# Kernel tuning notes

Hardware: AMD Instinct MI355X
Metric: run time of the kernel (lower is better)

The kernel has to match this reference:

```python
import jax, jax.numpy as jnp
import numpy as np

NEG_SLOPE = 0.2  # PyG GATConv default negative_slope


def gat_conv(x, edge_index, W, att_src, att_dst, bias):
    # PyG GATConv, heads=1, add_self_loops=True, lin bias=False, final bias added
    N = x.shape[0]
    h = x @ W                                     # [N, F]
    loops = jnp.arange(N, dtype=edge_index.dtype)
    src = jnp.concatenate([edge_index[0], loops])
    dst = jnp.concatenate([edge_index[1], loops])
    a_src = h @ att_src                           # [N]
    a_dst = h @ att_dst                           # [N]
    e = a_src[src] + a_dst[dst]
    e = jnp.where(e > 0, e, NEG_SLOPE * e)        # leaky_relu
    m = jax.ops.segment_max(e, dst, num_segments=N)
    w = jnp.exp(e - m[dst])
    denom = jax.ops.segment_sum(w, dst, num_segments=N)
    alpha = w / denom[dst]
    out = jax.ops.segment_sum(h[src] * alpha[:, None], dst, num_segments=N)
    return out + bias


def gcn_conv(x, edge_index, W, b):
    # PyG GCNConv: add self-loops + symmetric normalization
    N = x.shape[0]
    loops = jnp.arange(N, dtype=edge_index.dtype)
    src = jnp.concatenate([edge_index[0], loops])
    dst = jnp.concatenate([edge_index[1], loops])
    deg = jax.ops.segment_sum(jnp.ones(src.shape[0], dtype=x.dtype), dst, num_segments=N)
    dinv = jax.lax.rsqrt(jnp.maximum(deg, 1e-12))  # deg >= 1 thanks to self-loops
    norm = dinv[src] * dinv[dst]
    xw = x @ W
    return jax.ops.segment_sum(xw[src] * norm[:, None], dst, num_segments=N) + b


def get_final_node(x, batch, num_graphs):
    nn_ = jax.ops.segment_sum(jnp.ones(x.shape[0], dtype=jnp.int32), batch, num_segments=num_graphs)
    cum = jnp.concatenate([jnp.zeros(1, dtype=nn_.dtype), jnp.cumsum(nn_)[:-1]])
    return x[cum]


def ontology_emb(table, e1, e2, W, asrc, adst, b, idx_map):
    emb = gat_conv(table, e1, W, asrc, adst, b)
    emb = gat_conv(emb, e2, W, asrc, adst, b)
    return emb[idx_map]


def _forward(spec_emb, diag_table, proce_table, atc_table,
             diag_W, diag_asrc, diag_adst, diag_b,
             proce_W, proce_asrc, proce_adst, proce_b,
             atc_W, atc_asrc, atc_adst, atc_b,
             gcn_W1, gcn_b1, gcn_W2, gcn_b2, gcn_W3, gcn_b3,
             diag_e1, diag_e2, proce_e1, proce_e2, atc_e1, atc_e2,
             diag_map, proce_map, atc_map,
             left_x, left_graph_index, right_x, right_graph_index,
             left_x_batch, right_x_batch, num_graphs):
    diag_emb = ontology_emb(diag_table, diag_e1, diag_e2, diag_W, diag_asrc, diag_adst, diag_b, diag_map)
    proce_emb = ontology_emb(proce_table, proce_e1, proce_e2, proce_W, proce_asrc, proce_adst, proce_b, proce_map)
    atc_emb = ontology_emb(atc_table, atc_e1, atc_e2, atc_W, atc_asrc, atc_adst, atc_b, atc_map)
    all_emb = jnp.concatenate([spec_emb, diag_emb, proce_emb, atc_emb], axis=0)
    lh = all_emb[left_x[:, 0]]   # squeeze(dim=1)
    rh = all_emb[right_x[:, 0]]
    for W, b in ((gcn_W1, gcn_b1), (gcn_W2, gcn_b2), (gcn_W3, gcn_b3)):
        lh = gcn_conv(lh, left_graph_index, W, b)
        rh = gcn_conv(rh, right_graph_index, W, b)
    lf = get_final_node(lh, left_x_batch, num_graphs)
    rf = get_final_node(rh, right_x_batch, num_graphs)
    eps = 1e-6  # CosineSimilarity eps
    num = jnp.sum(lf * rf, axis=-1)
    den = jnp.maximum(jnp.linalg.norm(lf, axis=-1), eps) * jnp.maximum(jnp.linalg.norm(rf, axis=-1), eps)
    return num / den


def setup_inputs() -> dict:
    key = jax.random.key(0)
    ks = jax.random.split(key, 32)
    HID = 128
    B, NPG = 2048, 50
    N = B * NPG               # 102400 nodes per side
    E_PAT = 409600            # 4 edges per node
    DIAG_N, DIAG_L = 30000, 20000
    PROCE_N, PROCE_L = 12000, 8000
    ATC_N, ATC_L = 6000, 4000
    ALL = 1 + DIAG_L + PROCE_L + ATC_L
    f = lambda k, s: jax.random.normal(k, s, dtype=jnp.float32)
    scale = 0.1
    inp = {
        'spec_emb': f(ks[0], (1, HID)),
        'diag_table': f(ks[1], (DIAG_N, HID)),
        'proce_table': f(ks[2], (PROCE_N, HID)),
        'atc_table': f(ks[3], (ATC_N, HID)),
    }
    for i, nm in enumerate(['diag', 'proce', 'atc']):
        inp[nm + '_W'] = f(ks[4 + i], (HID, HID)) * scale
        inp[nm + '_asrc'] = f(ks[7 + i], (HID,)) * scale
        inp[nm + '_adst'] = f(ks[10 + i], (HID,)) * scale
        inp[nm + '_b'] = jnp.zeros((HID,), jnp.float32)
    for j in range(3):
        inp['gcn_W%d' % (j + 1)] = f(ks[13 + j], (HID, HID)) * scale
        inp['gcn_b%d' % (j + 1)] = jnp.zeros((HID,), jnp.float32)
    inp['diag_e1'] = jax.random.randint(ks[16], (2, DIAG_N), 0, DIAG_N, dtype=jnp.int32)
    inp['diag_e2'] = jax.random.randint(ks[17], (2, DIAG_N), 0, DIAG_N, dtype=jnp.int32)
    inp['proce_e1'] = jax.random.randint(ks[18], (2, PROCE_N), 0, PROCE_N, dtype=jnp.int32)
    inp['proce_e2'] = jax.random.randint(ks[19], (2, PROCE_N), 0, PROCE_N, dtype=jnp.int32)
    inp['atc_e1'] = jax.random.randint(ks[20], (2, ATC_N), 0, ATC_N, dtype=jnp.int32)
    inp['atc_e2'] = jax.random.randint(ks[21], (2, ATC_N), 0, ATC_N, dtype=jnp.int32)
    inp['diag_map'] = jnp.arange(DIAG_L, dtype=jnp.int32)
    inp['proce_map'] = jnp.arange(PROCE_L, dtype=jnp.int32)
    inp['atc_map'] = jnp.arange(ATC_L, dtype=jnp.int32)
    inp['left_x'] = jax.random.randint(ks[22], (N, 1), 0, ALL, dtype=jnp.int32)
    inp['right_x'] = jax.random.randint(ks[23], (N, 1), 0, ALL, dtype=jnp.int32)
    inp['left_graph_index'] = jax.random.randint(ks[24], (2, E_PAT), 0, N, dtype=jnp.int32)
    inp['right_graph_index'] = jax.random.randint(ks[25], (2, E_PAT), 0, N, dtype=jnp.int32)
    batch = jnp.repeat(jnp.arange(B, dtype=jnp.int32), NPG)
    inp['left_x_batch'] = batch
    inp['right_x_batch'] = batch
    inp['num_graphs'] = B
    return inp


def reference(spec_emb, diag_table, proce_table, atc_table,
              diag_W, diag_asrc, diag_adst, diag_b,
              proce_W, proce_asrc, proce_adst, proce_b,
              atc_W, atc_asrc, atc_adst, atc_b,
              gcn_W1, gcn_b1, gcn_W2, gcn_b2, gcn_W3, gcn_b3,
              diag_e1, diag_e2, proce_e1, proce_e2, atc_e1, atc_e2,
              diag_map, proce_map, atc_map,
              left_x, left_graph_index, right_x, right_graph_index,
              left_x_batch, right_x_batch, num_graphs):
    return _forward(spec_emb, diag_table, proce_table, atc_table,
                    diag_W, diag_asrc, diag_adst, diag_b,
                    proce_W, proce_asrc, proce_adst, proce_b,
                    atc_W, atc_asrc, atc_adst, atc_b,
                    gcn_W1, gcn_b1, gcn_W2, gcn_b2, gcn_W3, gcn_b3,
                    diag_e1, diag_e2, proce_e1, proce_e2, atc_e1, atc_e2,
                    diag_map, proce_map, atc_map,
                    left_x, left_graph_index, right_x, right_graph_index,
                    left_x_batch, right_x_batch, num_graphs)
```

## Files before the change

### kernel.cpp

```cpp
#include <hip/hip_runtime.h>
#include <hip/hip_bf16.h>

#define HID 128

typedef unsigned int uint;
typedef unsigned short ushort;
typedef short short8 __attribute__((ext_vector_type(8)));
typedef float f32x4 __attribute__((ext_vector_type(4)));

static inline int cdiv_i(long a, long b) { return (int)((a + b - 1) / b); }
static inline int imax_i(int a, int b) { return a > b ? a : b; }

__device__ __forceinline__ float bf2f(uint hi) {
    return __builtin_bit_cast(float, hi << 16);
}
__device__ __forceinline__ ushort f2bf(float f) {
    uint u = __builtin_bit_cast(uint, f);
    u = (u + 0x7fffu + ((u >> 16) & 1u)) >> 16;
    return (ushort)u;
}

struct CsrDesc {
    const int* esrc[8];
    const int* edst[8];
    int ebase[9];
    int nbase[9];
    int totE;
};

__device__ __forceinline__ void stage_wt(const ushort* __restrict__ Wt,
                                         ushort* __restrict__ wl) {
    const int t = threadIdx.x;
    const int row = t >> 1, half = (t & 1) * 64;
    const uint4* src = (const uint4*)(Wt + row * 128 + half);
    uint4* dst = (uint4*)(wl + row * 136 + half);
#pragma unroll
    for (int i = 0; i < 8; ++i) dst[i] = src[i];
}

template <typename AT>
__device__ __forceinline__ void load_afrag(const AT* __restrict__ A, long row,
                                           int koff, short8& af) {
    if constexpr (__is_same(AT, ushort)) {
        const uint4 raw = *(const uint4*)(A + row * 128 + koff);
        af = __builtin_bit_cast(short8, raw);
    } else {
        const float4* p = (const float4*)(A + row * 128 + koff);
        const float4 x0 = p[0], x1 = p[1];
        af[0] = (short)f2bf(x0.x); af[1] = (short)f2bf(x0.y);
        af[2] = (short)f2bf(x0.z); af[3] = (short)f2bf(x0.w);
        af[4] = (short)f2bf(x1.x); af[5] = (short)f2bf(x1.y);
        af[6] = (short)f2bf(x1.z); af[7] = (short)f2bf(x1.w);
    }
}

struct GOnto {
    const ushort* Wt0; const ushort* Wt1; const ushort* Wt2;
    const float* s0; const float* s1; const float* s2;
    const float* d0; const float* d1; const float* d2;
    int bs1, bs2;
    int r1, r2, r3;
};

template <typename AT>
__device__ void gemm_onto_dev(int b, const AT* __restrict__ x0,
                              const AT* __restrict__ x1, const AT* __restrict__ x2,
                              const GOnto& g, ushort* __restrict__ H,
                              float* __restrict__ as_o, float* __restrict__ ad_o,
                              ushort* __restrict__ wl) {
    const int gid = (b >= g.bs1) + (b >= g.bs2);
    const ushort* Wt = (gid == 0) ? g.Wt0 : (gid == 1) ? g.Wt1 : g.Wt2;
    const float* avs = (gid == 0) ? g.s0 : (gid == 1) ? g.s1 : g.s2;
    const float* avd = (gid == 0) ? g.d0 : (gid == 1) ? g.d1 : g.d2;
    const AT* Ag = (gid == 0) ? x0 : (gid == 1) ? x1 : x2;
    const int bloc = b - ((gid == 0) ? 0 : (gid == 1) ? g.bs1 : g.bs2);
    const long rb = (gid == 0) ? 0 : (gid == 1) ? g.r1 : g.r2;
    const long Mg = ((gid == 0) ? g.r1 : (gid == 1) ? g.r2 : g.r3) - rb;
    stage_wt(Wt, wl);
    __syncthreads();

    const int tid = threadIdx.x;
    const int wave = tid >> 6, lane = tid & 63;
    const int r = lane & 15, q = lane >> 4;
    const long m0 = (long)bloc * 128 + wave * 32;

    f32x4 acc[2][8];
#pragma unroll
    for (int mi = 0; mi < 2; ++mi)
#pragma unroll
        for (int ni = 0; ni < 8; ++ni) acc[mi][ni] = (f32x4)0.f;

#pragma unroll
    for (int t = 0; t < 4; ++t) {
        const int koff = t * 32 + q * 8;
        short8 bfr[8];
#pragma unroll
        for (int ni = 0; ni < 8; ++ni) {
            const uint4 raw = *(const uint4*)(&wl[(ni * 16 + r) * 136 + koff]);
            bfr[ni] = __builtin_bit_cast(short8, raw);
        }
#pragma unroll
        for (int mi = 0; mi < 2; ++mi) {
            long row = m0 + mi * 16 + r;
            if (row >= Mg) row = Mg - 1;
            short8 af;
            load_afrag<AT>(Ag, row, koff, af);
#pragma unroll
            for (int ni = 0; ni < 8; ++ni)
                acc[mi][ni] = __builtin_amdgcn_mfma_f32_16x16x32_bf16(
                    af, bfr[ni], acc[mi][ni], 0, 0, 0);
        }
    }

    ushort* Hg = H + rb * 128;
#pragma unroll
    for (int mi = 0; mi < 2; ++mi) {
#pragma unroll
        for (int ni = 0; ni < 8; ++ni) {
            const int col = ni * 16 + r;
#pragma unroll
            for (int reg = 0; reg < 4; ++reg) {
                const long row = m0 + mi * 16 + q * 4 + reg;
                if (row < Mg) Hg[row * 128 + col] = f2bf(acc[mi][ni][reg]);
            }
        }
    }

    float asv[8], adv[8];
#pragma unroll
    for (int ni = 0; ni < 8; ++ni) {
        asv[ni] = avs[ni * 16 + r];
        adv[ni] = avd[ni * 16 + r];
    }
#pragma unroll
    for (int mi = 0; mi < 2; ++mi) {
#pragma unroll
        for (int reg = 0; reg < 4; ++reg) {
            float ps = 0.f, pd = 0.f;
#pragma unroll
            for (int ni = 0; ni < 8; ++ni) {
                ps += acc[mi][ni][reg] * asv[ni];
                pd += acc[mi][ni][reg] * adv[ni];
            }
#pragma unroll
            for (int o = 1; o < 16; o <<= 1) {
                ps += __shfl_xor(ps, o);
                pd += __shfl_xor(pd, o);
            }
            const long row = m0 + mi * 16 + q * 4 + reg;
            if (r == 0 && row < Mg) {
                as_o[rb + row] = ps;
                ad_o[rb + row] = pd;
            }
        }
    }
}

__global__ __launch_bounds__(256) void gemm_onto_l2(const ushort* __restrict__ x0,
                                                    const ushort* __restrict__ x1,
                                                    const ushort* __restrict__ x2,
                                                    GOnto g, ushort* __restrict__ H,
                                                    float* __restrict__ as_o,
                                                    float* __restrict__ ad_o) {
    __shared__ ushort wl[128 * 136];
    gemm_onto_dev<ushort>(blockIdx.x, x0, x1, x2, g, H, as_o, ad_o, wl);
}

struct EmbSrc {
    const float* spec; const ushort* oE;
    const int* m0; const int* m1; const int* m2;
    int lb2, lb3, r1, r2;
};

__device__ __forceinline__ short8 load_emb(const EmbSrc& e, long row, int koff) {
    short8 af;
    if (row == 0) {
        const float4* pp = (const float4*)(e.spec + koff);
        const float4 x0 = pp[0], x1 = pp[1];
        af[0] = (short)f2bf(x0.x); af[1] = (short)f2bf(x0.y);
        af[2] = (short)f2bf(x0.z); af[3] = (short)f2bf(x0.w);
        af[4] = (short)f2bf(x1.x); af[5] = (short)f2bf(x1.y);
        af[6] = (short)f2bf(x1.z); af[7] = (short)f2bf(x1.w);
        return af;
    }
    const int r = (int)row;
    const int seg = (r >= e.lb2) + (r >= e.lb3);
    const int local = r - ((seg == 0) ? 1 : (seg == 1) ? e.lb2 : e.lb3);
    const int* mp = (seg == 0) ? e.m0 : (seg == 1) ? e.m1 : e.m2;
    const int rb = (seg == 0) ? 0 : (seg == 1) ? e.r1 : e.r2;
    const long sr = (long)rb + mp[local];
    return __builtin_bit_cast(short8, *(const uint4*)(e.oE + sr * 128 + koff));
}

__device__ void gemm_pat_tile(const EmbSrc& es, const ushort* __restrict__ wl,
                              ushort* __restrict__ C, long m0blk, long rowEnd) {
    const int tid = threadIdx.x;
    const int wave = tid >> 6, lane = tid & 63;
    const int r = lane & 15, q = lane >> 4;
    const long m0 = m0blk + wave * 32;

    f32x4 acc[2][8];
#pragma unroll
    for (int mi = 0; mi < 2; ++mi)
#pragma unroll
        for (int ni = 0; ni < 8; ++ni) acc[mi][ni] = (f32x4)0.f;

#pragma unroll
    for (int t = 0; t < 4; ++t) {
        const int koff = t * 32 + q * 8;
        short8 bfr[8];
#pragma unroll
        for (int ni = 0; ni < 8; ++ni) {
            const uint4 raw = *(const uint4*)(&wl[(ni * 16 + r) * 136 + koff]);
            bfr[ni] = __builtin_bit_cast(short8, raw);
        }
#pragma unroll
        for (int mi = 0; mi < 2; ++mi) {
            long row = m0 + mi * 16 + r;
            if (row >= rowEnd) row = rowEnd - 1;
            const short8 af = load_emb(es, row, koff);
#pragma unroll
            for (int ni = 0; ni < 8; ++ni)
                acc[mi][ni] = __builtin_amdgcn_mfma_f32_16x16x32_bf16(
                    af, bfr[ni], acc[mi][ni], 0, 0, 0);
        }
    }

#pragma unroll
    for (int mi = 0; mi < 2; ++mi) {
#pragma unroll
        for (int ni = 0; ni < 8; ++ni) {
            const int col = ni * 16 + r;
#pragma unroll
            for (int reg = 0; reg < 4; ++reg) {
                const long row = m0 + mi * 16 + q * 4 + reg;
                if (row < rowEnd) C[row * 128 + col] = f2bf(acc[mi][ni][reg]);
            }
        }
    }
}

__global__ __launch_bounds__(256) void gemm_pat(EmbSrc es,
                                                const ushort* __restrict__ Wt,
                                                ushort* __restrict__ C, int M) {
    __shared__ ushort wl[128 * 136];
    stage_wt(Wt, wl);
    __syncthreads();
    const long m0 = (long)blockIdx.x * 256;
    gemm_pat_tile(es, wl, C, m0, M);
    if (m0 + 128 < M) gemm_pat_tile(es, wl, C, m0 + 128, M);
}

__device__ __forceinline__ void fold1_dev(int idx, const float* __restrict__ W2,
                                          const float* __restrict__ b2,
                                          const float* __restrict__ W3,
                                          float* __restrict__ W23b) {
    if (idx >= 129 * 128) return;
    const int i = idx >> 7, j = idx & 127;
    const float* a = (i < 128) ? (W2 + i * 128) : b2;
    float s = 0.f;
#pragma unroll 8
    for (int k = 0; k < 128; ++k) s += a[k] * W3[k * 128 + j];
    W23b[idx] = s;
}

__device__ __forceinline__ void fold2_dev(int idx, const float* __restrict__ W1,
                                          const float* __restrict__ b1,
                                          const float* __restrict__ W23b,
                                          ushort* __restrict__ WpT,
                                          float* __restrict__ cbuf) {
    if (idx >= 130 * 128) return;
    const int i = idx >> 7, j = idx & 127;
    if (i == 129) { cbuf[128 + j] = W23b[128 * 128 + j]; return; }
    const float* a = (i < 128) ? (W1 + i * 128) : b1;
    float s = 0.f;
#pragma unroll 8
    for (int k = 0; k < 128; ++k) s += a[k] * W23b[k * 128 + j];
    if (i < 128) WpT[j * 128 + i] = f2bf(s);
    else cbuf[j] = s;
}

__device__ __forceinline__ void mark_dev(int i, const int* __restrict__ lEg,
                                         const int* __restrict__ rEg, int EP,
                                         int NP, int* __restrict__ mk,
                                         int testBit, int setBit) {
    int src, dst;
    if (i < 2 * EP) {
        const int side = i >= EP;
        const int e = i - side * EP;
        const int* eg = side ? rEg : lEg;
        src = side * NP + eg[e];
        dst = side * NP + eg[EP + e];
    } else if (i < 2 * EP + 2 * NP) {
        src = dst = i - 2 * EP;
    } else return;
    if (mk[dst] & testBit) atomicOr(&mk[src], setBit);
}

__device__ __forceinline__ void csr_count_dev(int i, const CsrDesc& d,
                                              int* __restrict__ cnt,
                                              int* __restrict__ pos) {
    if (i >= d.totE) return;
    int li = 0;
#pragma unroll
    for (int k = 1; k < 8; ++k) li += (i >= d.ebase[k]);
    const int v = d.nbase[li] + d.edst[li][i - d.ebase[li]];
    pos[i] = atomicAdd(&cnt[v], 1);
}

struct PackPrep {
    const float* W2; const float* b2; const float* W3; float* W23b;
    const float* wsrc[3]; ushort* wt_out;
    int* cnt; int NV;
    const int* bL; const int* bR; int NP;
    int* gfL; int* gfR; int* mk;
    int nbF1, nbWT, nbInit;
};

__global__ __launch_bounds__(256) void k_prep(PackPrep p) {
    const int b = blockIdx.x, tid = threadIdx.x;
    if (b < p.nbF1) {
        fold1_dev(b * 256 + tid, p.W2, p.b2, p.W3, p.W23b);
    } else if (b < p.nbF1 + p.nbWT) {
        const int idx = (b - p.nbF1) * 256 + tid;
        if (idx < 3 * 16384) {
            const int m = idx >> 14;
            const int e = idx & 16383;
            const int n = e >> 7, k = e & 127;
            p.wt_out[idx] = f2bf(p.wsrc[m][k * 128 + n]);
        }
    } else {
        const int i = (b - p.nbF1 - p.nbWT) * 256 + tid;
        if (i < p.NV) p.cnt[i] = 0;
        if (i < 2 * p.NP) {
            const int side = i >= p.NP;
            const int ii = i - (side ? p.NP : 0);
            const int* bb = side ? p.bR : p.bL;
            int* gf = side ? p.gfR : p.gfL;
            const int cur = bb[ii];
            const int prev = (ii == 0) ? -1 : bb[ii - 1];
            int m = 0;
            if (cur > prev) {
                for (int g = prev + 1; g <= cur; ++g) gf[g] = ii;
                m = 1;
            }
            p.mk[i] = m;
        }
    }
}

struct PackScatter {
    const float* W1; const float* b1; const float* W23b;
    ushort* WpT; float* cbuf;
    CsrDesc dsc; int* cnt; int* pos;
    const int* lEg; const int* rEg; int EP; int NP; int* mk;
    int nbF2, nbCnt, nbMark;
};

__global__ __launch_bounds__(256) void k_scatter(PackScatter p) {
    const int b = blockIdx.x, tid = threadIdx.x;
    if (b < p.nbF2) {
        fold2_dev(b * 256 + tid, p.W1, p.b1, p.W23b, p.WpT, p.cbuf);
    } else if (b < p.nbF2 + p.nbCnt) {
        csr_count_dev((b - p.nbF2) * 256 + tid, p.dsc, p.cnt, p.pos);
    } else {
        mark_dev((b - p.nbF2 - p.nbCnt) * 256 + tid, p.lEg, p.rEg, p.EP, p.NP,
                 p.mk, 1, 2);
    }
}

__device__ void scan_tile_dev(const int* __restrict__ in, int* __restrict__ out,
                              int* __restrict__ bsum, int n, int pn0, int pcnt,
                              float* __restrict__ dinv, int tb, int tid,
                              int* sbuf) {
    const int base = tb * 1024 + tid * 4;
    int v[4];
    int s = 0;
#pragma unroll
    for (int k = 0; k < 4; ++k) {
        const int i = base + k;
        v[k] = (i < n) ? (in[i] + 1) : 0;
        if (i >= pn0 && i < pn0 + pcnt)
            dinv[i - pn0] = rsqrtf(fmaxf((float)v[k], 1e-12f));
        s += v[k];
    }
    sbuf[tid] = s;
    __syncthreads();
    int x = s;
    for (int o = 1; o < 256; o <<= 1) {
        const int t = (tid >= o) ? sbuf[tid - o] : 0;
        __syncthreads();
        x += t;
        sbuf[tid] = x;
        __syncthreads();
    }
    int run = x - s;
#pragma unroll
    for (int k = 0; k < 4; ++k) {
        const int i = base + k;
        if (i < n) out[i] = run;
        run += v[k];
    }
    if (tid == 255) bsum[tb] = x;
}

struct PackMid {
    const float* x0; const float* x1; const float* x2;
    GOnto go; ushort* H; float* as_o; float* ad_o;
    const int* cnt; int* offs; int* bsum;
    int NV; int pn0; int pcnt; float* dinv;
    const int* lEg; const int* rEg; int EP; int NP; int* mk;
    int nbGemm, nbScan;
};

__global__ __launch_bounds__(256) void k_mid(PackMid p) {
    __shared__ uint smem4[128 * 136 / 2];
    const int b = blockIdx.x, tid = threadIdx.x;
    if (b < p.nbGemm) {
        gemm_onto_dev<float>(b, p.x0, p.x1, p.x2, p.go, p.H, p.as_o, p.ad_o,
                             (ushort*)smem4);
    } else if (b < p.nbGemm + p.nbScan) {
        scan_tile_dev(p.cnt, p.offs, p.bsum, p.NV, p.pn0, p.pcnt, p.dinv,
                      b - p.nbGemm, tid, (int*)smem4);
    } else {
        mark_dev((b - p.nbGemm - p.nbScan) * 256 + tid, p.lEg, p.rEg, p.EP,
                 p.NP, p.mk, 2, 4);
    }
}

__global__ __launch_bounds__(256) void k_scanfin(int* __restrict__ out,
                                                 const int* __restrict__ bsum,
                                                 int n, int nbData) {
    __shared__ int sbuf[256];
    const int tb = blockIdx.x, tid = threadIdx.x;
    int pLim = tb < nbData ? tb : nbData;
    int pth = 0;
    for (int j = tid; j < pLim; j += 256) pth += bsum[j];
    sbuf[tid] = pth;
    __syncthreads();
    for (int o = 128; o > 0; o >>= 1) {
        if (tid < o) sbuf[tid] += sbuf[tid + o];
        __syncthreads();
    }
    const int prefix = sbuf[0];
    const int base = tb * 1024 + tid * 4;
#pragma unroll
    for (int k = 0; k < 4; ++k) {
        const int i = base + k;
        if (i < n) out[i] += prefix;
        else if (i == n) out[i] = prefix + ((tb < nbData) ? bsum[tb] : 0);
    }
}

struct FillP {
    CsrDesc dsc;
    const int* offs; const int* pos; const int* cnt;
    int* srcl; int4* pedge; const float* dinv;
    const int* lx; const int* rx; const int* mk;
    int NP, pB;
    int eStart, eCount, vStart, vCount;
};

__device__ void fill_dev(const FillP& f, int idx) {
    int v, s, li, cidx;
    if (idx < f.eCount) {
        const int i = f.eStart + idx;
        li = 0;
#pragma unroll
        for (int k = 1; k < 8; ++k) li += (i >= f.dsc.ebase[k]);
        const int j = i - f.dsc.ebase[li];
        v = f.dsc.nbase[li] + f.dsc.edst[li][j];
        s = f.dsc.esrc[li][j];
        cidx = f.offs[v] + f.pos[i];
    } else if (idx < f.eCount + f.vCount) {
        v = f.vStart + (idx - f.eCount);
        li = 0;
#pragma unroll
        for (int k = 1; k < 8; ++k) li += (v >= f.dsc.nbase[k]);
        s = v - f.dsc.nbase[li];
        cidx = f.offs[v] + f.cnt[v];
    } else return;
    if (li >= 6) {
        const int n2l = v - f.dsc.nbase[6];
        if (f.mk[n2l] == 0) return;
        const int sg = (li - 6) * f.NP + s;
        int4 rec;
        rec.x = sg;
        rec.y = (li == 7 ? f.rx : f.lx)[s];
        rec.z = __float_as_int(f.dinv[n2l] * f.dinv[sg]);
        rec.w = 0;
        f.pedge[cidx - f.pB] = rec;
    } else {
        f.srcl[cidx] = s;
    }
}

__global__ __launch_bounds__(256) void k_fill(FillP f) {
    fill_dev(f, blockIdx.x * 256 + threadIdx.x);
}

struct GatP {
    int r1, r2;
    int ob0, ob1, ob2;
    const float* b0; const float* b1; const float* b2;
};

__device__ __forceinline__ void acc8(float* acc, float w, const uint4 v) {
    acc[0] += w * bf2f(v.x & 0xffff);
    acc[1] += w * bf2f(v.x >> 16);
    acc[2] += w * bf2f(v.y & 0xffff);
    acc[3] += w * bf2f(v.y >> 16);
    acc[4] += w * bf2f(v.z & 0xffff);
    acc[5] += w * bf2f(v.z >> 16);
    acc[6] += w * bf2f(v.w & 0xffff);
    acc[7] += w * bf2f(v.w >> 16);
}

__device__ void gat_dev(int node, int ql, const ushort* __restrict__ h,
                        const float* __restrict__ as, const float* __restrict__ ad,
                        const int* __restrict__ offs, const int* __restrict__ srcl,
                        const GatP& p, ushort* __restrict__ out, int Mtot) {
    if (node >= Mtot) return;
    const int gid = (node >= p.r1) + (node >= p.r2);
    const int rb = (gid == 0) ? 0 : (gid == 1) ? p.r1 : p.r2;
    const int ob = (gid == 0) ? p.ob0 : (gid == 1) ? p.ob1 : p.ob2;
    const float* bias = (gid == 0) ? p.b0 : (gid == 1) ? p.b1 : p.b2;
    const int local = node - rb;
    const int beg = offs[ob + local], end = offs[ob + local + 1];
    const float adv = ad[node];
    float m = -1e30f;
    for (int j = beg; j < end; ++j) {
        float e = as[rb + srcl[j]] + adv;
        e = (e > 0.f) ? e : 0.2f * e;
        m = fmaxf(m, e);
    }
    float denom = 0.f;
    float acc[8] = {0.f, 0.f, 0.f, 0.f, 0.f, 0.f, 0.f, 0.f};
    int j = beg;
    for (; j + 2 <= end; j += 2) {
        const int s0 = srcl[j], s1 = srcl[j + 1];
        float e0 = as[rb + s0] + adv; e0 = (e0 > 0.f) ? e0 : 0.2f * e0;
        float e1 = as[rb + s1] + adv; e1 = (e1 > 0.f) ? e1 : 0.2f * e1;
        const float w0 = __expf(e0 - m), w1 = __expf(e1 - m);
        const uint4 v0 = *(const uint4*)(h + (size_t)(rb + s0) * 128 + ql * 8);
        const uint4 v1 = *(const uint4*)(h + (size_t)(rb + s1) * 128 + ql * 8);
        denom += w0 + w1;
        acc8(acc, w0, v0);
        acc8(acc, w1, v1);
    }
    if (j < end) {
        const int s0 = srcl[j];
        float e0 = as[rb + s0] + adv; e0 = (e0 > 0.f) ? e0 : 0.2f * e0;
        const float w0 = __expf(e0 - m);
        const uint4 v0 = *(const uint4*)(h + (size_t)(rb + s0) * 128 + ql * 8);
        denom += w0;
        acc8(acc, w0, v0);
    }
    const float inv = 1.f / denom;
    const float4 bv0 = *(const float4*)(bias + ql * 8);
    const float4 bv1 = *(const float4*)(bias + ql * 8 + 4);
    uint4 o;
    o.x = (uint)f2bf(acc[0] * inv + bv0.x) | ((uint)f2bf(acc[1] * inv + bv0.y) << 16);
    o.y = (uint)f2bf(acc[2] * inv + bv0.z) | ((uint)f2bf(acc[3] * inv + bv0.w) << 16);
    o.z = (uint)f2bf(acc[4] * inv + bv1.x) | ((uint)f2bf(acc[5] * inv + bv1.y) << 16);
    o.w = (uint)f2bf(acc[6] * inv + bv1.z) | ((uint)f2bf(acc[7] * inv + bv1.w) << 16);
    *(uint4*)(out + (size_t)node * 128 + ql * 8) = o;
}

__global__ __launch_bounds__(256) void gat_all(const ushort* __restrict__ h,
                                               const float* __restrict__ as,
                                               const float* __restrict__ ad,
                                               const int* __restrict__ offs,
                                               const int* __restrict__ srcl,
                                               GatP p, ushort* __restrict__ out,
                                               int Mtot) {
    gat_dev(blockIdx.x * 16 + (threadIdx.x >> 4), threadIdx.x & 15, h, as, ad,
            offs, srcl, p, out, Mtot);
}

struct GatFill {
    const ushort* h; const float* as; const float* ad;
    const int* offs; const int* srcl;
    GatP gp; ushort* out; int Mtot; int nbGat;
    FillP f;
};

__global__ __launch_bounds__(256) void k_gat_fill(GatFill g) {
    const int b = blockIdx.x, tid = threadIdx.x;
    if (b < g.nbGat) {
        gat_dev(b * 16 + (tid >> 4), tid & 15, g.h, g.as, g.ad, g.offs, g.srcl,
                g.gp, g.out, g.Mtot);
    } else {
        fill_dev(g.f, (b - g.nbGat) * 256 + tid);
    }
}

__global__ __launch_bounds__(256) void gcn_agg1(const ushort* __restrict__ A3,
                                                const int4* __restrict__ pedge,
                                                const int* __restrict__ offs6,
                                                const float* __restrict__ c1,
                                                ushort* __restrict__ t1,
                                                const int* __restrict__ mk,
                                                int NP2, int pB) {
    const int n2 = blockIdx.x * 16 + (threadIdx.x >> 4);
    const int ql = threadIdx.x & 15;
    if (n2 >= NP2) return;
    if ((mk[n2] & 4) == 0) return;
    const int beg = offs6[n2] - pB, end = offs6[n2 + 1] - pB;
    float acc[8] = {0.f, 0.f, 0.f, 0.f, 0.f, 0.f, 0.f, 0.f};
    int j = beg;
    for (; j + 2 <= end; j += 2) {
        const int4 r0 = pedge[j], r1 = pedge[j + 1];
        const float w0 = __int_as_float(r0.z), w1 = __int_as_float(r1.z);
        const uint4 v0 = *(const uint4*)(A3 + (size_t)r0.y * 128 + ql * 8);
        const uint4 v1 = *(const uint4*)(A3 + (size_t)r1.y * 128 + ql * 8);
        acc8(acc, w0, v0);
        acc8(acc, w1, v1);
    }
    if (j < end) {
        const int4 r0 = pedge[j];
        const uint4 v0 = *(const uint4*)(A3 + (size_t)r0.y * 128 + ql * 8);
        acc8(acc, __int_as_float(r0.z), v0);
    }
    const float4 bv0 = *(const float4*)(c1 + ql * 8);
    const float4 bv1 = *(const float4*)(c1 + ql * 8 + 4);
    uint4 o;
    o.x = (uint)f2bf(acc[0] + bv0.x) | ((uint)f2bf(acc[1] + bv0.y) << 16);
    o.y = (uint)f2bf(acc[2] + bv0.z) | ((uint)f2bf(acc[3] + bv0.w) << 16);
    o.z = (uint)f2bf(acc[4] + bv1.x) | ((uint)f2bf(acc[5] + bv1.y) << 16);
    o.w = (uint)f2bf(acc[6] + bv1.z) | ((uint)f2bf(acc[7] + bv1.w) << 16);
    *(uint4*)(t1 + (size_t)n2 * 128 + ql * 8) = o;
}

__device__ __forceinline__ void gcn_q_acc(const ushort* __restrict__ x,
                                          const int4* __restrict__ pedge,
                                          int beg, int end, int ql, float* acc) {
    int j = beg;
    for (; j + 2 <= end; j += 2) {
        const int4 r0 = pedge[j], r1 = pedge[j + 1];
        const float w0 = __int_as_float(r0.z), w1 = __int_as_float(r1.z);
        const uint4 v0 = *(const uint4*)(x + (size_t)r0.x * 128 + ql * 8);
        const uint4 v1 = *(const uint4*)(x + (size_t)r1.x * 128 + ql * 8);
        acc8(acc, w0, v0);
        acc8(acc, w1, v1);
    }
    if (j < end) {
        const int4 r0 = pedge[j];
        const uint4 v0 = *(const uint4*)(x + (size_t)r0.x * 128 + ql * 8);
        acc8(acc, __int_as_float(r0.z), v0);
    }
}

__global__ __launch_bounds__(256) void gcn_agg2(const ushort* __restrict__ t1,
                                                const int4* __restrict__ pedge,
                                                const int* __restrict__ offs6,
                                                const float* __restrict__ c2,
                                                ushort* __restrict__ t2,
                                                const int* __restrict__ mk,
                                                int NP2, int pB) {
    const int n2 = blockIdx.x * 16 + (threadIdx.x >> 4);
    const int ql = threadIdx.x & 15;
    if (n2 >= NP2) return;
    if ((mk[n2] & 2) == 0) return;
    const int beg = offs6[n2] - pB, end = offs6[n2 + 1] - pB;
    float acc[8] = {0.f, 0.f, 0.f, 0.f, 0.f, 0.f, 0.f, 0.f};
    gcn_q_acc(t1, pedge, beg, end, ql, acc);
    const float4 bv0 = *(const float4*)(c2 + ql * 8);
    const float4 bv1 = *(const float4*)(c2 + ql * 8 + 4);
    uint4 o;
    o.x = (uint)f2bf(acc[0] + bv0.x) | ((uint)f2bf(acc[1] + bv0.y) << 16);
    o.y = (uint)f2bf(acc[2] + bv0.z) | ((uint)f2bf(acc[3] + bv0.w) << 16);
    o.z = (uint)f2bf(acc[4] + bv1.x) | ((uint)f2bf(acc[5] + bv1.y) << 16);
    o.w = (uint)f2bf(acc[6] + bv1.z) | ((uint)f2bf(acc[7] + bv1.w) << 16);
    *(uint4*)(t2 + (size_t)n2 * 128 + ql * 8) = o;
}

__global__ __launch_bounds__(256) void final_cos(const ushort* __restrict__ t2,
                                                 const int4* __restrict__ pedge,
                                                 const int* __restrict__ offs6,
                                                 const int* __restrict__ gfL,
                                                 const int* __restrict__ gfR,
                                                 const float* __restrict__ b3,
                                                 float* __restrict__ out,
                                                 int B, int NP, int pB) {
    const int g = blockIdx.x * 8 + (threadIdx.x >> 5);
    const int l32 = threadIdx.x & 31;
    const int side = l32 >> 4;
    const int ql = l32 & 15;
    if (g >= B) return;
    const int n2 = (side ? NP : 0) + (side ? gfR : gfL)[g];
    const int beg = offs6[n2] - pB, end = offs6[n2 + 1] - pB;
    float acc[8] = {0.f, 0.f, 0.f, 0.f, 0.f, 0.f, 0.f, 0.f};
    gcn_q_acc(t2, pedge, beg, end, ql, acc);
    const float4 bv0 = *(const float4*)(b3 + ql * 8);
    const float4 bv1 = *(const float4*)(b3 + ql * 8 + 4);
    float v[8];
    v[0] = acc[0] + bv0.x; v[1] = acc[1] + bv0.y;
    v[2] = acc[2] + bv0.z; v[3] = acc[3] + bv0.w;
    v[4] = acc[4] + bv1.x; v[5] = acc[5] + bv1.y;
    v[6] = acc[6] + bv1.z; v[7] = acc[7] + bv1.w;
    float num = 0.f, nself = 0.f, nother = 0.f;
#pragma unroll
    for (int j = 0; j < 8; ++j) {
        const float o = __shfl_xor(v[j], 16);
        num += v[j] * o;
        nself += v[j] * v[j];
        nother += o * o;
    }
#pragma unroll
    for (int o1 = 1; o1 < 16; o1 <<= 1) {
        num += __shfl_xor(num, o1);
        nself += __shfl_xor(nself, o1);
        nother += __shfl_xor(nother, o1);
    }
    if (l32 == 0)
        out[g] = num / (fmaxf(sqrtf(nself), 1e-6f) * fmaxf(sqrtf(nother), 1e-6f));
}

extern "C" void kernel_launch(void* const* d_in, const int* in_sizes, int n_in,
                              void* d_out, int out_size, void* d_ws, size_t ws_size,
                              hipStream_t stream) {
    (void)n_in; (void)ws_size;
    const float* spec = (const float*)d_in[0];
    const float* tabs[3] = {(const float*)d_in[1], (const float*)d_in[2], (const float*)d_in[3]};
    const float* ontW[3] = {(const float*)d_in[4], (const float*)d_in[8], (const float*)d_in[12]};
    const float* ontAs[3] = {(const float*)d_in[5], (const float*)d_in[9], (const float*)d_in[13]};
    const float* ontAd[3] = {(const float*)d_in[6], (const float*)d_in[10], (const float*)d_in[14]};
    const float* ontB[3] = {(const float*)d_in[7], (const float*)d_in[11], (const float*)d_in[15]};
    const float* gcnW[3] = {(const float*)d_in[16], (const float*)d_in[18], (const float*)d_in[20]};
    const float* gcnB[3] = {(const float*)d_in[17], (const float*)d_in[19], (const float*)d_in[21]};
    const int* e1s[3] = {(const int*)d_in[22], (const int*)d_in[24], (const int*)d_in[26]};
    const int* e2s[3] = {(const int*)d_in[23], (const int*)d_in[25], (const int*)d_in[27]};
    const int* maps[3] = {(const int*)d_in[28], (const int*)d_in[29], (const int*)d_in[30]};
    const int* left_x = (const int*)d_in[31];
    const int* right_x = (const int*)d_in[32];
    const int* left_eg = (const int*)d_in[33];
    const int* right_eg = (const int*)d_in[34];
    const int* left_batch = (const int*)d_in[35];
    const int* right_batch = (const int*)d_in[36];

    int Ms[3] = {in_sizes[1] / HID, in_sizes[2] / HID, in_sizes[3] / HID};
    int E1s[3] = {in_sizes[22] / 2, in_sizes[24] / 2, in_sizes[26] / 2};
    int E2s[3] = {in_sizes[23] / 2, in_sizes[25] / 2, in_sizes[27] / 2};
    int Ls[3] = {in_sizes[28], in_sizes[29], in_sizes[30]};
    const int NP = in_sizes[31];
    const int EP = in_sizes[33] / 2;
    const int B = out_size;
    const long ALL = 1 + (long)Ls[0] + Ls[1] + Ls[2];
    const int Mtot = Ms[0] + Ms[1] + Ms[2];
    const int r1 = Ms[0], r2 = Ms[0] + Ms[1];

    CsrDesc dsc;
    int eCnt[8], nCnt[8];
    for (int i = 0; i < 3; ++i) {
        dsc.esrc[2 * i] = e1s[i];     dsc.edst[2 * i] = e1s[i] + E1s[i];
        dsc.esrc[2 * i + 1] = e2s[i]; dsc.edst[2 * i + 1] = e2s[i] + E2s[i];
        eCnt[2 * i] = E1s[i]; eCnt[2 * i + 1] = E2s[i];
        nCnt[2 * i] = Ms[i];  nCnt[2 * i + 1] = Ms[i];
    }
    dsc.esrc[6] = left_eg;  dsc.edst[6] = left_eg + EP;  eCnt[6] = EP; nCnt[6] = NP;
    dsc.esrc[7] = right_eg; dsc.edst[7] = right_eg + EP; eCnt[7] = EP; nCnt[7] = NP;
    dsc.ebase[0] = 0;
    int nb_acc = 0;
    for (int i = 0; i < 8; ++i) {
        dsc.ebase[i + 1] = dsc.ebase[i] + eCnt[i];
        dsc.nbase[i] = nb_acc;
        nb_acc += nCnt[i];
    }
    const int NV = nb_acc;
    dsc.nbase[8] = NV;
    dsc.totE = dsc.ebase[8];
    const int totEntries = dsc.totE + NV;
    const int pB = dsc.ebase[6] + dsc.nbase[6];
    const int pEntries = totEntries - pB;

    char* ws = (char*)d_ws;
    size_t off = 0;
    auto alloc = [&](size_t bytes) -> void* {
        off = (off + 255) & ~(size_t)255;
        void* p = ws + off;
        off += bytes;
        return p;
    };
    ushort* wt4 = (ushort*)alloc((size_t)4 * 16384 * 2);
    float* W23b = (float*)alloc((size_t)129 * 128 * 4);
    float* cbuf = (float*)alloc((size_t)256 * 4);
    ushort* A3 = (ushort*)alloc((size_t)ALL * HID * 2);
    int* cnt = (int*)alloc((size_t)NV * 4);
    int* offs = (int*)alloc((size_t)(NV + 1) * 4);
    int* pos = (int*)alloc((size_t)dsc.totE * 4);
    int* srcl = (int*)alloc((size_t)pB * 4);
    int4* pedge = (int4*)alloc((size_t)pEntries * 16);
    int* bsum = (int*)alloc(1025 * 4);
    float* dinv = (float*)alloc((size_t)2 * NP * 4);
    float* as = (float*)alloc((size_t)Mtot * 4);
    float* ad = (float*)alloc((size_t)Mtot * 4);
    int* gfL = (int*)alloc((size_t)(B + 1) * 4);
    int* gfR = (int*)alloc((size_t)(B + 1) * 4);
    int* mk = (int*)alloc((size_t)2 * NP * 4);
    ushort* t1 = (ushort*)alloc((size_t)2 * NP * HID * 2);
    ushort* big = (ushort*)alloc((size_t)2 * NP * HID * 2);
    ushort* hbuf = big;
    ushort* obuf = big + (size_t)Mtot * HID;
    ushort* t2 = big;

    const ushort* wtOnt[3] = {wt4, wt4 + 16384, wt4 + 2 * 16384};
    ushort* WpT = wt4 + 3 * 16384;
    const float* c1 = cbuf;
    const float* c2 = cbuf + 128;

    PackPrep pp;
    pp.W2 = gcnW[1]; pp.b2 = gcnB[1]; pp.W3 = gcnW[2]; pp.W23b = W23b;
    pp.wsrc[0] = ontW[0]; pp.wsrc[1] = ontW[1]; pp.wsrc[2] = ontW[2];
    pp.wt_out = wt4;
    pp.cnt = cnt; pp.NV = NV;
    pp.bL = left_batch; pp.bR = right_batch; pp.NP = NP;
    pp.gfL = gfL; pp.gfR = gfR; pp.mk = mk;
    pp.nbF1 = cdiv_i(129 * 128, 256);
    pp.nbWT = cdiv_i(3 * 16384, 256);
    pp.nbInit = cdiv_i(imax_i(NV, 2 * NP), 256);
    k_prep<<<pp.nbF1 + pp.nbWT + pp.nbInit, 256, 0, stream>>>(pp);

    GOnto go;
    go.Wt0 = wtOnt[0]; go.Wt1 = wtOnt[1]; go.Wt2 = wtOnt[2];
    go.s0 = ontAs[0]; go.s1 = ontAs[1]; go.s2 = ontAs[2];
    go.d0 = ontAd[0]; go.d1 = ontAd[1]; go.d2 = ontAd[2];
    go.bs1 = cdiv_i(Ms[0], 128);
    go.bs2 = go.bs1 + cdiv_i(Ms[1], 128);
    const int totBlk = go.bs2 + cdiv_i(Ms[2], 128);
    go.r1 = r1; go.r2 = r2; go.r3 = Mtot;

    PackScatter psc;
    psc.W1 = gcnW[0]; psc.b1 = gcnB[0]; psc.W23b = W23b;
    psc.WpT = WpT; psc.cbuf = cbuf;
    psc.dsc = dsc; psc.cnt = cnt; psc.pos = pos;
    psc.lEg = left_eg; psc.rEg = right_eg; psc.EP = EP; psc.NP = NP; psc.mk = mk;
    psc.nbF2 = cdiv_i(130 * 128, 256);
    psc.nbCnt = cdiv_i(dsc.totE, 256);
    psc.nbMark = cdiv_i(2 * EP + 2 * NP, 256);
    k_scatter<<<psc.nbF2 + psc.nbCnt + psc.nbMark, 256, 0, stream>>>(psc);

    PackMid pm;
    pm.x0 = tabs[0]; pm.x1 = tabs[1]; pm.x2 = tabs[2];
    pm.go = go; pm.H = hbuf; pm.as_o = as; pm.ad_o = ad;
    pm.cnt = cnt; pm.offs = offs; pm.bsum = bsum;
    pm.NV = NV; pm.pn0 = dsc.nbase[6]; pm.pcnt = 2 * NP; pm.dinv = dinv;
    pm.lEg = left_eg; pm.rEg = right_eg; pm.EP = EP; pm.NP = NP; pm.mk = mk;
    pm.nbGemm = totBlk;
    pm.nbScan = cdiv_i(NV, 1024);
    k_mid<<<pm.nbGemm + pm.nbScan + psc.nbMark, 256, 0, stream>>>(pm);

    k_scanfin<<<cdiv_i(NV + 1, 1024), 256, 0, stream>>>(offs, bsum, NV, pm.nbScan);

    FillP fb;
    fb.dsc = dsc; fb.offs = offs; fb.pos = pos; fb.cnt = cnt;
    fb.srcl = srcl; fb.pedge = pedge; fb.dinv = dinv;
    fb.lx = left_x; fb.rx = right_x; fb.mk = mk;
    fb.NP = NP; fb.pB = pB;

    FillP fo = fb;
    fo.eStart = 0;             fo.eCount = dsc.ebase[6];
    fo.vStart = 0;             fo.vCount = dsc.nbase[6];
    k_fill<<<cdiv_i(fo.eCount + fo.vCount, 256), 256, 0, stream>>>(fo);

    GatFill gf;
    gf.h = hbuf; gf.as = as; gf.ad = ad; gf.offs = offs; gf.srcl = srcl;
    gf.gp = GatP{r1, r2, dsc.nbase[0], dsc.nbase[2], dsc.nbase[4],
                 ontB[0], ontB[1], ontB[2]};
    gf.out = obuf; gf.Mtot = Mtot;
    gf.nbGat = cdiv_i(Mtot, 16);
    gf.f = fb;
    gf.f.eStart = dsc.ebase[6]; gf.f.eCount = dsc.totE - dsc.ebase[6];
    gf.f.vStart = dsc.nbase[6]; gf.f.vCount = NV - dsc.nbase[6];
    k_gat_fill<<<gf.nbGat + cdiv_i(gf.f.eCount + gf.f.vCount, 256), 256, 0,
                 stream>>>(gf);

    gemm_onto_l2<<<totBlk, 256, 0, stream>>>(obuf, obuf + (size_t)r1 * HID,
                                             obuf + (size_t)r2 * HID, go, hbuf,
                                             as, ad);
    const GatP gp1{r1, r2, dsc.nbase[1], dsc.nbase[3], dsc.nbase[5],
                   ontB[0], ontB[1], ontB[2]};
    gat_all<<<cdiv_i(Mtot, 16), 256, 0, stream>>>(hbuf, as, ad, offs, srcl, gp1,
                                                  obuf, Mtot);

    EmbSrc es;
    es.spec = spec; es.oE = obuf;
    es.m0 = maps[0]; es.m1 = maps[1]; es.m2 = maps[2];
    es.lb2 = 1 + Ls[0]; es.lb3 = 1 + Ls[0] + Ls[1];
    es.r1 = r1; es.r2 = r2;
    gemm_pat<<<cdiv_i(ALL, 256), 256, 0, stream>>>(es, WpT, A3, (int)ALL);

    const int* offs6 = offs + dsc.nbase[6];
    gcn_agg1<<<cdiv_i(2 * NP, 16), 256, 0, stream>>>(A3, pedge, offs6, c1, t1,
                                                     mk, 2 * NP, pB);
    gcn_agg2<<<cdiv_i(2 * NP, 16), 256, 0, stream>>>(t1, pedge, offs6, c2, t2,
                                                     mk, 2 * NP, pB);
    final_cos<<<cdiv_i(B, 8), 256, 0, stream>>>(t2, pedge, offs6, gfL, gfR,
                                                gcnB[2], (float*)d_out, B, NP, pB);
}
```

Before: 360.9 us.

## Read GEMM weights from global memory and merge ontology GEMM into scatter kernel

Removes LDS staging of the transposed weight matrix in the ontology and patient GEMMs, so B fragments are loaded directly from global memory (served by cache). Without the large shared-memory allocation, the ontology GEMM blocks can be fused into the earlier scatter/count/fold launch, and the scan runs in a lighter kernel with a small LDS buffer. This cuts the __syncthreads staging cost and raises occupancy. The trade-off is repeated global or L2 reads of weights per wave, with no padding against bank conflicts.

Result: no change. 360.9 us (+0.0%).

```diff
diff --git a/kernel.cpp b/kernel.cpp
--- a/kernel.cpp
+++ b/kernel.cpp
@@ -27,16 +27,6 @@
     int nbase[9];
     int totE;
 };
-
-__device__ __forceinline__ void stage_wt(const ushort* __restrict__ Wt,
-                                         ushort* __restrict__ wl) {
-    const int t = threadIdx.x;
-    const int row = t >> 1, half = (t & 1) * 64;
-    const uint4* src = (const uint4*)(Wt + row * 128 + half);
-    uint4* dst = (uint4*)(wl + row * 136 + half);
-#pragma unroll
-    for (int i = 0; i < 8; ++i) dst[i] = src[i];
-}
 
 template <typename AT>
 __device__ __forceinline__ void load_afrag(const AT* __restrict__ A, long row,
@@ -66,8 +56,7 @@
 __device__ void gemm_onto_dev(int b, const AT* __restrict__ x0,
                               const AT* __restrict__ x1, const AT* __restrict__ x2,
                               const GOnto& g, ushort* __restrict__ H,
-                              float* __restrict__ as_o, float* __restrict__ ad_o,
-                              ushort* __restrict__ wl) {
+                              float* __restrict__ as_o, float* __restrict__ ad_o) {
     const int gid = (b >= g.bs1) + (b >= g.bs2);
     const ushort* Wt = (gid == 0) ? g.Wt0 : (gid == 1) ? g.Wt1 : g.Wt2;
     const float* avs = (gid == 0) ? g.s0 : (gid == 1) ? g.s1 : g.s2;
@@ -76,8 +65,6 @@
     const int bloc = b - ((gid == 0) ? 0 : (gid == 1) ? g.bs1 : g.bs2);
     const long rb = (gid == 0) ? 0 : (gid == 1) ? g.r1 : g.r2;
     const long Mg = ((gid == 0) ? g.r1 : (gid == 1) ? g.r2 : g.r3) - rb;
-    stage_wt(Wt, wl);
-    __syncthreads();
 
     const int tid = threadIdx.x;
     const int wave = tid >> 6, lane = tid & 63;
@@ -96,7 +83,7 @@
         short8 bfr[8];
 #pragma unroll
         for (int ni = 0; ni < 8; ++ni) {
-            const uint4 raw = *(const uint4*)(&wl[(ni * 16 + r) * 136 + koff]);
+            const uint4 raw = *(const uint4*)(Wt + (ni * 16 + r) * 128 + koff);
             bfr[ni] = __builtin_bit_cast(short8, raw);
         }
 #pragma unroll
@@ -162,8 +149,7 @@
                                                     GOnto g, ushort* __restrict__ H,
                                                     float* __restrict__ as_o,
                                                     float* __restrict__ ad_o) {
-    __shared__ ushort wl[128 * 136];
-    gemm_onto_dev<ushort>(blockIdx.x, x0, x1, x2, g, H, as_o, ad_o, wl);
+    gemm_onto_dev<ushort>(blockIdx.x, x0, x1, x2, g, H, as_o, ad_o);
 }
 
 struct EmbSrc {
@@ -192,7 +178,7 @@
     return __builtin_bit_cast(short8, *(const uint4*)(e.oE + sr * 128 + koff));
 }
 
-__device__ void gemm_pat_tile(const EmbSrc& es, const ushort* __restrict__ wl,
+__device__ void gemm_pat_tile(const EmbSrc& es, const ushort* __restrict__ Wt,
                               ushort* __restrict__ C, long m0blk, long rowEnd) {
     const int tid = threadIdx.x;
     const int wave = tid >> 6, lane = tid & 63;
@@ -211,7 +197,7 @@
         short8 bfr[8];
 #pragma unroll
         for (int ni = 0; ni < 8; ++ni) {
-            const uint4 raw = *(const uint4*)(&wl[(ni * 16 + r) * 136 + koff]);
+            const uint4 raw = *(const uint4*)(Wt + (ni * 16 + r) * 128 + koff);
             bfr[ni] = __builtin_bit_cast(short8, raw);
         }
 #pragma unroll
@@ -243,12 +229,9 @@
 __global__ __launch_bounds__(256) void gemm_pat(EmbSrc es,
                                                 const ushort* __restrict__ Wt,
                                                 ushort* __restrict__ C, int M) {
-    __shared__ ushort wl[128 * 136];
-    stage_wt(Wt, wl);
-    __syncthreads();
     const long m0 = (long)blockIdx.x * 256;
-    gemm_pat_tile(es, wl, C, m0, M);
-    if (m0 + 128 < M) gemm_pat_tile(es, wl, C, m0 + 128, M);
+    gemm_pat_tile(es, Wt, C, m0, M);
+    if (m0 + 128 < M) gemm_pat_tile(es, Wt, C, m0 + 128, M);
 }
 
 __device__ __forceinline__ void fold1_dev(int idx, const float* __restrict__ W2,
@@ -349,23 +332,27 @@
     }
 }
 
-struct PackScatter {
+struct PackBig {
+    const float* x0; const float* x1; const float* x2;
+    GOnto go; ushort* H; float* as_o; float* ad_o;
     const float* W1; const float* b1; const float* W23b;
     ushort* WpT; float* cbuf;
     CsrDesc dsc; int* cnt; int* pos;
     const int* lEg; const int* rEg; int EP; int NP; int* mk;
-    int nbF2, nbCnt, nbMark;
+    int nbGemm, nbF2, nbCnt;
 };
 
-__global__ __launch_bounds__(256) void k_scatter(PackScatter p) {
+__global__ __launch_bounds__(256) void k_big1(PackBig p) {
     const int b = blockIdx.x, tid = threadIdx.x;
-    if (b < p.nbF2) {
-        fold2_dev(b * 256 + tid, p.W1, p.b1, p.W23b, p.WpT, p.cbuf);
-    } else if (b < p.nbF2 + p.nbCnt) {
-        csr_count_dev((b - p.nbF2) * 256 + tid, p.dsc, p.cnt, p.pos);
+    if (b < p.nbGemm) {
+        gemm_onto_dev<float>(b, p.x0, p.x1, p.x2, p.go, p.H, p.as_o, p.ad_o);
+    } else if (b < p.nbGemm + p.nbF2) {
+        fold2_dev((b - p.nbGemm) * 256 + tid, p.W1, p.b1, p.W23b, p.WpT, p.cbuf);
+    } else if (b < p.nbGemm + p.nbF2 + p.nbCnt) {
+        csr_count_dev((b - p.nbGemm - p.nbF2) * 256 + tid, p.dsc, p.cnt, p.pos);
     } else {
-        mark_dev((b - p.nbF2 - p.nbCnt) * 256 + tid, p.lEg, p.rEg, p.EP, p.NP,
-                 p.mk, 1, 2);
+        mark_dev((b - p.nbGemm - p.nbF2 - p.nbCnt) * 256 + tid, p.lEg, p.rEg,
+                 p.EP, p.NP, p.mk, 1, 2);
     }
 }
 
@@ -404,27 +391,22 @@
     if (tid == 255) bsum[tb] = x;
 }
 
-struct PackMid {
-    const float* x0; const float* x1; const float* x2;
-    GOnto go; ushort* H; float* as_o; float* ad_o;
+struct PackScan {
     const int* cnt; int* offs; int* bsum;
     int NV; int pn0; int pcnt; float* dinv;
     const int* lEg; const int* rEg; int EP; int NP; int* mk;
-    int nbGemm, nbScan;
+    int nbScan;
 };
 
-__global__ __launch_bounds__(256) void k_mid(PackMid p) {
-    __shared__ uint smem4[128 * 136 / 2];
+__global__ __launch_bounds__(256) void k_scan(PackScan p) {
+    __shared__ int sbuf[256];
     const int b = blockIdx.x, tid = threadIdx.x;
-    if (b < p.nbGemm) {
-        gemm_onto_dev<float>(b, p.x0, p.x1, p.x2, p.go, p.H, p.as_o, p.ad_o,
-                             (ushort*)smem4);
-    } else if (b < p.nbGemm + p.nbScan) {
-        scan_tile_dev(p.cnt, p.offs, p.bsum, p.NV, p.pn0, p.pcnt, p.dinv,
-                      b - p.nbGemm, tid, (int*)smem4);
+    if (b < p.nbScan) {
+        scan_tile_dev(p.cnt, p.offs, p.bsum, p.NV, p.pn0, p.pcnt, p.dinv, b,
+                      tid, sbuf);
     } else {
-        mark_dev((b - p.nbGemm - p.nbScan) * 256 + tid, p.lEg, p.rEg, p.EP,
-                 p.NP, p.mk, 2, 4);
+        mark_dev((b - p.nbScan) * 256 + tid, p.lEg, p.rEg, p.EP, p.NP, p.mk,
+                 2, 4);
     }
 }
 
@@ -830,27 +812,27 @@
     const int totBlk = go.bs2 + cdiv_i(Ms[2], 128);
     go.r1 = r1; go.r2 = r2; go.r3 = Mtot;
 
-    PackScatter psc;
-    psc.W1 = gcnW[0]; psc.b1 = gcnB[0]; psc.W23b = W23b;
-    psc.WpT = WpT; psc.cbuf = cbuf;
-    psc.dsc = dsc; psc.cnt = cnt; psc.pos = pos;
-    psc.lEg = left_eg; psc.rEg = right_eg; psc.EP = EP; psc.NP = NP; psc.mk = mk;
-    psc.nbF2 = cdiv_i(130 * 128, 256);
-    psc.nbCnt = cdiv_i(dsc.totE, 256);
-    psc.nbMark = cdiv_i(2 * EP + 2 * NP, 256);
-    k_scatter<<<psc.nbF2 + psc.nbCnt + psc.nbMark, 256, 0, stream>>>(psc);
-
-    PackMid pm;
-    pm.x0 = tabs[0]; pm.x1 = tabs[1]; pm.x2 = tabs[2];
-    pm.go = go; pm.H = hbuf; pm.as_o = as; pm.ad_o = ad;
-    pm.cnt = cnt; pm.offs = offs; pm.bsum = bsum;
-    pm.NV = NV; pm.pn0 = dsc.nbase[6]; pm.pcnt = 2 * NP; pm.dinv = dinv;
-    pm.lEg = left_eg; pm.rEg = right_eg; pm.EP = EP; pm.NP = NP; pm.mk = mk;
-    pm.nbGemm = totBlk;
-    pm.nbScan = cdiv_i(NV, 1024);
-    k_mid<<<pm.nbGemm + pm.nbScan + psc.nbMark, 256, 0, stream>>>(pm);
-
-    k_scanfin<<<cdiv_i(NV + 1, 1024), 256, 0, stream>>>(offs, bsum, NV, pm.nbScan);
+    PackBig pg;
+    pg.x0 = tabs[0]; pg.x1 = tabs[1]; pg.x2 = tabs[2];
+    pg.go = go; pg.H = hbuf; pg.as_o = as; pg.ad_o = ad;
+    pg.W1 = gcnW[0]; pg.b1 = gcnB[0]; pg.W23b = W23b;
+    pg.WpT = WpT; pg.cbuf = cbuf;
+    pg.dsc = dsc; pg.cnt = cnt; pg.pos = pos;
+    pg.lEg = left_eg; pg.rEg = right_eg; pg.EP = EP; pg.NP = NP; pg.mk = mk;
+    pg.nbGemm = totBlk;
+    pg.nbF2 = cdiv_i(130 * 128, 256);
+    pg.nbCnt = cdiv_i(dsc.totE, 256);
+    const int nbMark = cdiv_i(2 * EP + 2 * NP, 256);
+    k_big1<<<pg.nbGemm + pg.nbF2 + pg.nbCnt + nbMark, 256, 0, stream>>>(pg);
+
+    PackScan psn;
+    psn.cnt = cnt; psn.offs = offs; psn.bsum = bsum;
+    psn.NV = NV; psn.pn0 = dsc.nbase[6]; psn.pcnt = 2 * NP; psn.dinv = dinv;
+    psn.lEg = left_eg; psn.rEg = right_eg; psn.EP = EP; psn.NP = NP; psn.mk = mk;
+    psn.nbScan = cdiv_i(NV, 1024);
+    k_scan<<<psn.nbScan + nbMark, 256, 0, stream>>>(psn);
+
+    k_scanfin<<<cdiv_i(NV + 1, 1024), 256, 0, stream>>>(offs, bsum, NV, psn.nbScan);
 
     FillP fb;
     fb.dsc = dsc; fb.offs = offs; fb.pos = pos; fb.cnt = cnt;
```
